# Kernel tuning notes

Hardware: AMD Instinct MI355X
Metric: run time of the kernel (lower is better)

Reference implementation:

```python
import jax, jax.numpy as jnp
import numpy as np

DECAY = 0.99
EPS = 1e-5
BETA = 0.25

def _l2norm(v, axis=-1):
    # F.normalize: x / max(||x||, 1e-12)
    n = jnp.sqrt(jnp.sum(v * v, axis=axis, keepdims=True))
    return v / jnp.maximum(n, 1e-12)

def setup_inputs() -> dict:
    key = jax.random.key(0)
    k0, k1, k2, k3 = jax.random.split(key, 4)
    B, C, H, W, E, K = 8, 256, 64, 64, 32, 8192
    x = jax.random.normal(k0, (B, C, H, W), jnp.float32)
    Wq = jax.random.normal(k1, (E, C), jnp.float32) * 0.05  # 1x1 conv kernel
    bq = jnp.zeros((E,), jnp.float32)
    emb = jax.random.normal(k2, (K, E), jnp.float32)
    emb = _l2norm(emb, axis=1)  # matches F.normalize init in __init__
    ema_cluster_size = jnp.ones((K,), jnp.float32)
    ema_weight = emb  # consistent post-init EMA state
    return {"x": x, "Wq": Wq, "bq": bq, "embedding": emb,
            "ema_cluster_size": ema_cluster_size, "ema_weight": ema_weight}

def reference(x, Wq, bq, embedding, ema_cluster_size, ema_weight):
    B, C, H, W = x.shape
    E = Wq.shape[0]
    K = embedding.shape[0]
    # quant_conv: 1x1 conv == per-pixel linear
    z = jnp.einsum('bchw,ec->behw', x, Wq) + bq[None, :, None, None]  # [B,E,H,W]
    z_flat = z.transpose(0, 2, 3, 1).reshape(-1, E)  # [N,E]
    # get_idx(use_znorm=True): cosine similarity argmax (== argmin L2 on normalized)
    zn = _l2norm(z_flat, axis=1)
    en = _l2norm(embedding, axis=1)
    indices = jnp.argmax(zn @ en.T, axis=1)  # [N]
    # codebook gather (raw embedding, as in torch)
    z_q = embedding[indices].reshape(B, H, W, E).transpose(0, 3, 1, 2)  # [B,E,H,W]
    # EMA update (training path; scatter == one-hot.T @ z_flat / one-hot.sum)
    counts = jax.ops.segment_sum(jnp.ones((z_flat.shape[0],), z_flat.dtype), indices, num_segments=K)
    dw = jax.ops.segment_sum(z_flat, indices, num_segments=K)  # [K,E]
    new_cs = DECAY * ema_cluster_size + (1.0 - DECAY) * counts
    new_w = DECAY * ema_weight + (1.0 - DECAY) * dw
    n = jnp.sum(new_cs)
    cs_smoothed = (new_cs + EPS) / (n + K * EPS) * n
    new_embedding = new_w / cs_smoothed[:, None]
    # commitment loss + straight-through
    qloss = BETA * jnp.mean((jax.lax.stop_gradient(z_q) - z) ** 2)
    z_q_st = z + jax.lax.stop_gradient(z_q - z)
    return (z_q_st, indices.reshape(B, H, W), qloss, new_embedding, new_cs, new_w)
```

## Files before the change

kernel.cpp:

```cpp
#include <hip/hip_runtime.h>

#define B_ 8
#define C_ 256
#define HW_ 4096
#define E_ 32
#define K_ 8192
#define N_ 32768
#define NCHUNK 4
#define KC_ (K_ / NCHUNK)
#define NSTAGE (KC_ / 128)
#define KSEG 32

#define DECAY_ 0.99f
#define OMD_   0.01f
#define EPS_   1e-5f
#define BETA_  0.25f

#define O_ZQ   0
#define O_IDX  1048576
#define O_QL   1081344
#define O_NEMB 1081345
#define O_NCS  1343489
#define O_NW   1351681

#define WS_EH   0u
#define WS_EM   131072u
#define WS_Z    262144u
#define WS_PACK 1310720u
#define WS_CNT  1572864u
#define WS_DW   1581056u
#define WS_SCAL 1843200u

typedef float f32x4 __attribute__((ext_vector_type(4)));
typedef short s16x8 __attribute__((ext_vector_type(8)));
typedef unsigned long long u64;

__device__ __forceinline__ unsigned short f2bf(float f) {
    unsigned u = __float_as_uint(f);
    u = u + 0x7fffu + ((u >> 16) & 1u);
    return (unsigned short)(u >> 16);
}
__device__ __forceinline__ float bf2f(unsigned short h) {
    return __uint_as_float(((unsigned)h) << 16);
}
__device__ __forceinline__ unsigned ford(float f) {
    unsigned u = __float_as_uint(f);
    return (u & 0x80000000u) ? ~u : (u | 0x80000000u);
}
__device__ __forceinline__ int imax(int a, int b) { return a > b ? a : b; }
__device__ __forceinline__ int imin(int a, int b) { return a < b ? a : b; }

__device__ __forceinline__ void gload_lds16(const void* g, void* l) {
    __builtin_amdgcn_global_load_lds(
        (const __attribute__((address_space(1))) unsigned int*)g,
        (__attribute__((address_space(3))) unsigned int*)l, 16, 0, 0);
}

__global__ __launch_bounds__(256) void k_norm_split(const float* __restrict__ emb,
                                                    uint4* __restrict__ eh16,
                                                    uint4* __restrict__ em16) {
    int k = blockIdx.x * 256 + threadIdx.x;
    if (k >= K_) return;
    const float4* r = (const float4*)(emb + (size_t)k * E_);
    float v[E_];
    float ss = 0.f;
#pragma unroll
    for (int i = 0; i < 8; i++) {
        float4 t = r[i];
        v[i*4+0] = t.x; v[i*4+1] = t.y; v[i*4+2] = t.z; v[i*4+3] = t.w;
        ss += t.x*t.x + t.y*t.y + t.z*t.z + t.w*t.w;
    }
    float inv = 1.0f / fmaxf(sqrtf(ss), 1e-12f);
    unsigned short h1a[E_], h2a[E_];
#pragma unroll
    for (int e = 0; e < E_; e++) {
        float en = v[e] * inv;
        unsigned short h1 = f2bf(en);
        float r1 = en - bf2f(h1);
        h1a[e] = h1; h2a[e] = f2bf(r1);
    }
    int t = k >> 4, c15 = k & 15;
#pragma unroll
    for (int i = 0; i < 4; i++) {
        eh16[t * 64 + i * 16 + c15] = ((uint4*)h1a)[i];
        em16[t * 64 + i * 16 + c15] = ((uint4*)h2a)[i];
    }
}

__global__ __launch_bounds__(512) void k_z(const float* __restrict__ x,
                                           const float* __restrict__ Wq,
                                           const float* __restrict__ bq,
                                           float* __restrict__ zout) {
    __shared__ float wqt[C_ * E_];
    int tid = threadIdx.x;
#pragma unroll
    for (int i = 0; i < 16; i++) {
        int g = i * 512 + tid;
        int e = g >> 8;
        int c = g & 255;
        wqt[c * E_ + e] = Wq[g];
    }
    __syncthreads();
    int lp = tid & 63, eg = tid >> 6;
    int n0 = blockIdx.x * 64 + lp;
    int b  = n0 >> 12, hw = n0 & (HW_ - 1);
    const float* xp = x + (size_t)b * C_ * HW_ + hw;
    float a0 = 0.f, a1 = 0.f, a2 = 0.f, a3 = 0.f;
#pragma unroll 4
    for (int c = 0; c < C_; c++) {
        float xv = xp[(size_t)c * HW_];
        float4 wv = *(const float4*)(wqt + c * E_ + eg * 4);
        a0 += xv * wv.x; a1 += xv * wv.y; a2 += xv * wv.z; a3 += xv * wv.w;
    }
    float4 o = make_float4(a0 + bq[eg*4+0], a1 + bq[eg*4+1],
                           a2 + bq[eg*4+2], a3 + bq[eg*4+3]);
    *(float4*)(zout + (size_t)n0 * E_ + eg * 4) = o;
}

__global__ __launch_bounds__(256, 4) void k_score_mfma(const float* __restrict__ zws,
                                                       const char* __restrict__ ehb,
                                                       const char* __restrict__ emb_b,
                                                       int2* __restrict__ pk2) {
    __shared__ __align__(16) char smem[32768];

    int tid  = threadIdx.x;
    int lane = tid & 63;
    int w    = tid >> 6;
    int chunk = blockIdx.y;

    s16x8 a1, a2;
    {
        int ploc = w * 16 + (lane & 15);
        int n0   = blockIdx.x * 64 + ploc;
        int e0   = (lane >> 4) * 8;
        const float4* zp = (const float4*)(zws + (size_t)n0 * E_ + e0);
        float4 z0 = zp[0], z1 = zp[1];
        float zz[8] = {z0.x, z0.y, z0.z, z0.w, z1.x, z1.y, z1.z, z1.w};
#pragma unroll
        for (int j = 0; j < 8; j++) {
            float zv = zz[j] * 134217728.0f;
            unsigned short h1 = f2bf(zv);
            float r1 = zv - bf2f(h1);
            a1[j] = (short)h1; a2[j] = (short)f2bf(r1);
        }
    }

    const char* srcp[4];
#pragma unroll
    for (int i = 0; i < 4; i++) {
        int d = i * 256 + tid;
        int pl = d >> 9, dd = d & 511;
        srcp[i] = (pl ? emb_b : ehb) + (size_t)chunk * (KC_ * 64) + dd * 16;
    }

#pragma unroll
    for (int i = 0; i < 4; i++)
        gload_lds16(srcp[i], smem + (i * 256 + tid) * 16);
    __syncthreads();

    int rbase = 8191 - chunk * KC_ - (lane & 15);
    int bq1[4], bq2[4];
#pragma unroll
    for (int j = 0; j < 4; j++) { bq1[j] = (int)0x80000000; bq2[j] = (int)0x80000000; }
    f32x4 zero4 = {0.f, 0.f, 0.f, 0.f};

    for (int st = 0; st < NSTAGE; st++) {
        if (st + 1 < NSTAGE) {
            char* dst = smem + ((st + 1) & 1) * 16384;
#pragma unroll
            for (int i = 0; i < 4; i++)
                gload_lds16(srcp[i] + (size_t)(st + 1) * 8192, dst + (i * 256 + tid) * 16);
        }
        const char* cur = smem + (st & 1) * 16384;
        int rst = rbase - st * 128;

#pragma unroll
        for (int g = 0; g < 2; g++) {
            int ct = g * 4;
            s16x8 b1[4], b2[4];
#pragma unroll
            for (int q = 0; q < 4; q++) {
                b1[q] = ((const s16x8*)(cur +        (ct + q) * 1024))[lane];
                b2[q] = ((const s16x8*)(cur + 8192 + (ct + q) * 1024))[lane];
            }
            f32x4 acc[4];
#pragma unroll
            for (int q = 0; q < 4; q++)
                acc[q] = __builtin_amdgcn_mfma_f32_16x16x32_bf16(a1, b1[q], zero4, 0, 0, 0);
#pragma unroll
            for (int q = 0; q < 4; q++)
                acc[q] = __builtin_amdgcn_mfma_f32_16x16x32_bf16(a1, b2[q], acc[q], 0, 0, 0);
#pragma unroll
            for (int q = 0; q < 4; q++)
                acc[q] = __builtin_amdgcn_mfma_f32_16x16x32_bf16(a2, b1[q], acc[q], 0, 0, 0);
            int r0 = rst - ct * 16;
#pragma unroll
            for (int j = 0; j < 4; j++) {
                int v0 = ((int)acc[0][j] & (int)0xFFFFE000) | r0;
                int v1 = ((int)acc[1][j] & (int)0xFFFFE000) | (r0 - 16);
                int v2 = ((int)acc[2][j] & (int)0xFFFFE000) | (r0 - 32);
                int v3 = ((int)acc[3][j] & (int)0xFFFFE000) | (r0 - 48);
                int hi = imax(imax(v0, v1), imax(v2, v3));
                int m  = imin(bq1[j], hi);
                bq1[j] = imax(bq1[j], hi);
                bq2[j] = imax(bq2[j], m);
            }
        }
        __syncthreads();
    }

#pragma unroll
    for (int off = 1; off < 16; off <<= 1) {
#pragma unroll
        for (int j = 0; j < 4; j++) {
            int o1 = __shfl_xor(bq1[j], off, 64);
            int o2 = __shfl_xor(bq2[j], off, 64);
            int m  = imin(bq1[j], o1);
            bq1[j] = imax(bq1[j], o1);
            bq2[j] = imax(imax(bq2[j], o2), m);
        }
    }
    if ((lane & 15) == 0) {
        int rowbase = blockIdx.x * 64 + w * 16 + (lane >> 4) * 4;
#pragma unroll
        for (int j = 0; j < 4; j++)
            pk2[(size_t)chunk * N_ + rowbase + j] = make_int2(bq1[j], bq2[j]);
    }
}

__device__ __forceinline__ float rescore(const float* __restrict__ emb, int k,
                                         const float* zrow) {
    const float4* r = (const float4*)(emb + (size_t)k * E_);
    float4 v[8];
    float ss = 0.f;
#pragma unroll
    for (int i = 0; i < 8; i++) {
        v[i] = r[i];
        ss += v[i].x * v[i].x + v[i].y * v[i].y + v[i].z * v[i].z + v[i].w * v[i].w;
    }
    float inv = 1.0f / fmaxf(sqrtf(ss), 1e-12f);
    const float4* zp = (const float4*)zrow;
    float sx = 0.f, sy = 0.f, sz = 0.f, sw = 0.f;
#pragma unroll
    for (int i = 0; i < 8; i++) {
        float4 e4 = make_float4(v[i].x * inv, v[i].y * inv, v[i].z * inv, v[i].w * inv);
        float4 zr = zp[i];
        sx += zr.x * e4.x; sy += zr.y * e4.y;
        sz += zr.z * e4.z; sw += zr.w * e4.w;
    }
    return (sx + sy) + (sz + sw);
}

__global__ __launch_bounds__(256) void k_scatter(const float* __restrict__ zws,
                                                 const int2* __restrict__ pk2,
                                                 const float* __restrict__ emb,
                                                 float* __restrict__ out_zq,
                                                 float* __restrict__ out_idx,
                                                 float* __restrict__ scal) {
    __shared__ float zbuf[64 * E_];
    __shared__ int   idxs_s[64];
    __shared__ float red[4];
    int tid = threadIdx.x;

    const float4* zsrc = (const float4*)(zws + (size_t)blockIdx.x * 64 * E_);
    float4* zdst = (float4*)zbuf;
    zdst[tid]       = zsrc[tid];
    zdst[tid + 256] = zsrc[tid + 256];
    __syncthreads();

    {
        int p = tid >> 2, c4 = tid & 3;
        int nn = blockIdx.x * 64 + p;
        int2 c2 = pk2[(size_t)c4 * N_ + nn];
        u64 pkd = 0;
#pragma unroll
        for (int t = 0; t < 2; t++) {
            int raw = t ? c2.y : c2.x;
            int k = 8191 - (raw & 0x1fff);
            k = k < 0 ? 0 : (k > K_ - 1 ? K_ - 1 : k);
            float s = rescore(emb, k, zbuf + p * E_);
            u64 pk = ((u64)ford(s) << 32) | (unsigned)(K_ - 1 - k);
            pkd = pkd > pk ? pkd : pk;
        }
        u64 o = __shfl_xor(pkd, 1, 64); pkd = pkd > o ? pkd : o;
        o = __shfl_xor(pkd, 2, 64);     pkd = pkd > o ? pkd : o;
        if (c4 == 0) {
            int bi = K_ - 1 - (int)(unsigned)(pkd & 0xffffffffu);
            idxs_s[p] = bi;
            out_idx[nn] = (float)bi;
        }
    }
    __syncthreads();

    int lp = tid & 63, eg = tid >> 6;
    int n  = blockIdx.x * 64 + lp;
    int b  = n >> 12, hw = n & (HW_ - 1);
    int idx = idxs_s[lp];
    const float* er = emb + (size_t)idx * E_ + eg * 8;
    float* o = out_zq + (size_t)b * E_ * HW_ + (size_t)(eg * 8) * HW_ + hw;

    float sq = 0.f;
#pragma unroll
    for (int j = 0; j < 8; j++) {
        float zv = zbuf[lp * E_ + eg * 8 + j];
        float qf = er[j];
        float d = qf - zv;
        sq += d * d;
        o[(size_t)j * HW_] = qf;
    }

#pragma unroll
    for (int off = 32; off > 0; off >>= 1) sq += __shfl_down(sq, off);
    int lane = tid & 63, wid = tid >> 6;
    if (lane == 0) red[wid] = sq;
    __syncthreads();
    if (tid == 0) atomicAdd(scal + 1, red[0] + red[1] + red[2] + red[3]);
}

__global__ __launch_bounds__(256) void k_dw(const float* __restrict__ zws,
                                            const float* __restrict__ idxf,
                                            float* __restrict__ dw,
                                            float* __restrict__ cnt) {
    __shared__ float acc[KSEG * E_];
    __shared__ int   cnt_s[KSEG];
    int tid = threadIdx.x;
    int kbase = blockIdx.x * KSEG;

#pragma unroll
    for (int i = 0; i < KSEG * E_ / 256; i++) acc[tid + i * 256] = 0.f;
    if (tid < KSEG) cnt_s[tid] = 0;
    __syncthreads();

    const float4* idx4 = (const float4*)idxf;
#pragma unroll 2
    for (int it = 0; it < N_ / 1024; ++it) {
        float4 f = idx4[it * 256 + tid];
        int n0 = (it * 256 + tid) * 4;
        int ii[4] = {(int)f.x, (int)f.y, (int)f.z, (int)f.w};
#pragma unroll
        for (int s = 0; s < 4; s++) {
            unsigned d = (unsigned)(ii[s] - kbase);
            if (d < (unsigned)KSEG) {
                const float4* zr = (const float4*)(zws + (size_t)(n0 + s) * E_);
                float* ap = acc + d * E_;
#pragma unroll
                for (int j = 0; j < 8; j++) {
                    float4 v = zr[j];
                    atomicAdd(ap + j * 4 + 0, v.x);
                    atomicAdd(ap + j * 4 + 1, v.y);
                    atomicAdd(ap + j * 4 + 2, v.z);
                    atomicAdd(ap + j * 4 + 3, v.w);
                }
                atomicAdd(cnt_s + d, 1);
            }
        }
    }
    __syncthreads();

#pragma unroll
    for (int i = 0; i < KSEG * E_ / 256; i++)
        dw[(size_t)kbase * E_ + tid + i * 256] = acc[tid + i * 256];
    if (tid < KSEG) cnt[kbase + tid] = (float)cnt_s[tid];
}

__global__ __launch_bounds__(256) void k_ema_cs(const float* __restrict__ cs,
                                                const float* __restrict__ cnt,
                                                float* __restrict__ out_ncs,
                                                float* __restrict__ scal) {
    int tid = threadIdx.x;
    int k = blockIdx.x * 256 + tid;
    float v = DECAY_ * cs[k] + OMD_ * cnt[k];
    out_ncs[k] = v;

    float s = v;
#pragma unroll
    for (int off = 32; off > 0; off >>= 1) s += __shfl_down(s, off);
    __shared__ float red[4];
    int lane = tid & 63, wid = tid >> 6;
    if (lane == 0) red[wid] = s;
    __syncthreads();
    if (tid == 0) atomicAdd(scal + 0, red[0] + red[1] + red[2] + red[3]);
}

__global__ __launch_bounds__(256) void k_final(const float* __restrict__ ew,
                                               const float* __restrict__ dw,
                                               const float* __restrict__ cs,
                                               const float* __restrict__ cnt,
                                               const float* __restrict__ scal,
                                               float* __restrict__ out_nw,
                                               float* __restrict__ out_nemb,
                                               float* __restrict__ out_ql) {
    int j = blockIdx.x * 256 + threadIdx.x;
    float v = DECAY_ * ew[j] + OMD_ * dw[j];
    out_nw[j] = v;
    float nsum = scal[0];
    int k = j >> 5;
    float csk = DECAY_ * cs[k] + OMD_ * cnt[k];
    float denom = (csk + EPS_) / (nsum + (float)K_ * EPS_) * nsum;
    out_nemb[j] = v / denom;
    if (j == 0) {
        out_ql[0] = BETA_ * scal[1] / (float)(B_ * E_ * HW_);
    }
}

extern "C" void kernel_launch(void* const* d_in, const int* in_sizes, int n_in,
                              void* d_out, int out_size, void* d_ws, size_t ws_size,
                              hipStream_t stream) {
    const float* x   = (const float*)d_in[0];
    const float* Wq  = (const float*)d_in[1];
    const float* bq  = (const float*)d_in[2];
    const float* emb = (const float*)d_in[3];
    const float* cs  = (const float*)d_in[4];
    const float* ew  = (const float*)d_in[5];
    float* out = (float*)d_out;
    float* ws  = (float*)d_ws;

    hipMemsetAsync(ws + WS_SCAL, 0, 2 * sizeof(float), stream);

    k_norm_split<<<K_ / 256, 256, 0, stream>>>(emb,
        (uint4*)(ws + WS_EH), (uint4*)(ws + WS_EM));
    k_z<<<N_ / 64, 512, 0, stream>>>(x, Wq, bq, ws + WS_Z);
    k_score_mfma<<<dim3(N_ / 64, NCHUNK), 256, 0, stream>>>(ws + WS_Z,
        (const char*)(ws + WS_EH), (const char*)(ws + WS_EM),
        (int2*)(ws + WS_PACK));
    k_scatter<<<N_ / 64, 256, 0, stream>>>(ws + WS_Z,
        (const int2*)(ws + WS_PACK), emb,
        out + O_ZQ, out + O_IDX, ws + WS_SCAL);
    k_dw<<<K_ / KSEG, 256, 0, stream>>>(ws + WS_Z, out + O_IDX,
                                        ws + WS_DW, ws + WS_CNT);
    k_ema_cs<<<K_ / 256, 256, 0, stream>>>(cs, ws + WS_CNT, out + O_NCS, ws + WS_SCAL);
    k_final<<<(K_ * E_) / 256, 256, 0, stream>>>(ew, ws + WS_DW, cs, ws + WS_CNT,
                                                 ws + WS_SCAL, out + O_NW,
                                                 out + O_NEMB, out + O_QL);
}
```

Before: 218.6 us.

## Enlarge score blocks to 512 threads, fold EMA cluster-size kernel into others

The scoring kernel now uses 512-thread blocks covering 128 pixels, so each staged codebook tile in shared memory is reused by twice as many waves and half as many blocks reload it. The separate EMA cluster-size kernel is removed. The sum of new cluster sizes is computed analytically from the sum of old sizes, accumulated in the norm kernel, plus the total pixel count, and k_final now writes the new cluster sizes. The norm kernel is also split across four threads per codebook row for more parallelism. Risks are lower occupancy from the larger blocks and tiny float differences in the analytic sum.

```diff
diff --git a/kernel.cpp b/kernel.cpp
--- a/kernel.cpp
+++ b/kernel.cpp
@@ -10,6 +10,7 @@
 #define KC_ (K_ / NCHUNK)
 #define NSTAGE (KC_ / 128)
 #define KSEG 32
+#define PIX 128
 
 #define DECAY_ 0.99f
 #define OMD_   0.01f
@@ -57,33 +58,38 @@
 }
 
 __global__ __launch_bounds__(256) void k_norm_split(const float* __restrict__ emb,
+                                                    const float* __restrict__ cs,
                                                     uint4* __restrict__ eh16,
-                                                    uint4* __restrict__ em16) {
-    int k = blockIdx.x * 256 + threadIdx.x;
-    if (k >= K_) return;
-    const float4* r = (const float4*)(emb + (size_t)k * E_);
-    float v[E_];
-    float ss = 0.f;
-#pragma unroll
-    for (int i = 0; i < 8; i++) {
-        float4 t = r[i];
-        v[i*4+0] = t.x; v[i*4+1] = t.y; v[i*4+2] = t.z; v[i*4+3] = t.w;
-        ss += t.x*t.x + t.y*t.y + t.z*t.z + t.w*t.w;
-    }
+                                                    uint4* __restrict__ em16,
+                                                    float* __restrict__ scal) {
+    int t4 = blockIdx.x * 256 + threadIdx.x;
+    int k = t4 >> 2, q = t4 & 3;
+    const float4* r = (const float4*)(emb + (size_t)k * E_ + q * 8);
+    float4 u0 = r[0], u1 = r[1];
+    float ss = u0.x*u0.x + u0.y*u0.y + u0.z*u0.z + u0.w*u0.w
+             + u1.x*u1.x + u1.y*u1.y + u1.z*u1.z + u1.w*u1.w;
+    ss += __shfl_xor(ss, 1, 64);
+    ss += __shfl_xor(ss, 2, 64);
     float inv = 1.0f / fmaxf(sqrtf(ss), 1e-12f);
-    unsigned short h1a[E_], h2a[E_];
-#pragma unroll
-    for (int e = 0; e < E_; e++) {
+
+    float v[8] = {u0.x, u0.y, u0.z, u0.w, u1.x, u1.y, u1.z, u1.w};
+    unsigned short h1a[8], h2a[8];
+#pragma unroll
+    for (int e = 0; e < 8; e++) {
         float en = v[e] * inv;
         unsigned short h1 = f2bf(en);
         float r1 = en - bf2f(h1);
         h1a[e] = h1; h2a[e] = f2bf(r1);
     }
     int t = k >> 4, c15 = k & 15;
-#pragma unroll
-    for (int i = 0; i < 4; i++) {
-        eh16[t * 64 + i * 16 + c15] = ((uint4*)h1a)[i];
-        em16[t * 64 + i * 16 + c15] = ((uint4*)h2a)[i];
+    eh16[t * 64 + q * 16 + c15] = ((uint4*)h1a)[0];
+    em16[t * 64 + q * 16 + c15] = ((uint4*)h2a)[0];
+
+    if (threadIdx.x < 64) {
+        float cv = cs[blockIdx.x * 64 + threadIdx.x];
+#pragma unroll
+        for (int off = 32; off > 0; off >>= 1) cv += __shfl_down(cv, off);
+        if (threadIdx.x == 0) atomicAdd(scal + 0, cv);
     }
 }
 
@@ -117,7 +123,7 @@
     *(float4*)(zout + (size_t)n0 * E_ + eg * 4) = o;
 }
 
-__global__ __launch_bounds__(256, 4) void k_score_mfma(const float* __restrict__ zws,
+__global__ __launch_bounds__(512, 8) void k_score_mfma(const float* __restrict__ zws,
                                                        const char* __restrict__ ehb,
                                                        const char* __restrict__ emb_b,
                                                        int2* __restrict__ pk2) {
@@ -131,7 +137,7 @@
     s16x8 a1, a2;
     {
         int ploc = w * 16 + (lane & 15);
-        int n0   = blockIdx.x * 64 + ploc;
+        int n0   = blockIdx.x * PIX + ploc;
         int e0   = (lane >> 4) * 8;
         const float4* zp = (const float4*)(zws + (size_t)n0 * E_ + e0);
         float4 z0 = zp[0], z1 = zp[1];
@@ -145,17 +151,17 @@
         }
     }
 
-    const char* srcp[4];
-#pragma unroll
-    for (int i = 0; i < 4; i++) {
-        int d = i * 256 + tid;
+    const char* srcp[2];
+#pragma unroll
+    for (int i = 0; i < 2; i++) {
+        int d = i * 512 + tid;
         int pl = d >> 9, dd = d & 511;
         srcp[i] = (pl ? emb_b : ehb) + (size_t)chunk * (KC_ * 64) + dd * 16;
     }
 
 #pragma unroll
-    for (int i = 0; i < 4; i++)
-        gload_lds16(srcp[i], smem + (i * 256 + tid) * 16);
+    for (int i = 0; i < 2; i++)
+        gload_lds16(srcp[i], smem + (i * 512 + tid) * 16);
     __syncthreads();
 
     int rbase = 8191 - chunk * KC_ - (lane & 15);
@@ -168,8 +174,8 @@
         if (st + 1 < NSTAGE) {
             char* dst = smem + ((st + 1) & 1) * 16384;
 #pragma unroll
-            for (int i = 0; i < 4; i++)
-                gload_lds16(srcp[i] + (size_t)(st + 1) * 8192, dst + (i * 256 + tid) * 16);
+            for (int i = 0; i < 2; i++)
+                gload_lds16(srcp[i] + (size_t)(st + 1) * 8192, dst + (i * 512 + tid) * 16);
         }
         const char* cur = smem + (st & 1) * 16384;
         int rst = rbase - st * 128;
@@ -221,7 +227,7 @@
         }
     }
     if ((lane & 15) == 0) {
-        int rowbase = blockIdx.x * 64 + w * 16 + (lane >> 4) * 4;
+        int rowbase = blockIdx.x * PIX + w * 16 + (lane >> 4) * 4;
 #pragma unroll
         for (int j = 0; j < 4; j++)
             pk2[(size_t)chunk * N_ + rowbase + j] = make_int2(bq1[j], bq2[j]);
@@ -363,25 +369,6 @@
     if (tid < KSEG) cnt[kbase + tid] = (float)cnt_s[tid];
 }
 
-__global__ __launch_bounds__(256) void k_ema_cs(const float* __restrict__ cs,
-                                                const float* __restrict__ cnt,
-                                                float* __restrict__ out_ncs,
-                                                float* __restrict__ scal) {
-    int tid = threadIdx.x;
-    int k = blockIdx.x * 256 + tid;
-    float v = DECAY_ * cs[k] + OMD_ * cnt[k];
-    out_ncs[k] = v;
-
-    float s = v;
-#pragma unroll
-    for (int off = 32; off > 0; off >>= 1) s += __shfl_down(s, off);
-    __shared__ float red[4];
-    int lane = tid & 63, wid = tid >> 6;
-    if (lane == 0) red[wid] = s;
-    __syncthreads();
-    if (tid == 0) atomicAdd(scal + 0, red[0] + red[1] + red[2] + red[3]);
-}
-
 __global__ __launch_bounds__(256) void k_final(const float* __restrict__ ew,
                                                const float* __restrict__ dw,
                                                const float* __restrict__ cs,
@@ -389,15 +376,17 @@
                                                const float* __restrict__ scal,
                                                float* __restrict__ out_nw,
                                                float* __restrict__ out_nemb,
+                                               float* __restrict__ out_ncs,
                                                float* __restrict__ out_ql) {
     int j = blockIdx.x * 256 + threadIdx.x;
     float v = DECAY_ * ew[j] + OMD_ * dw[j];
     out_nw[j] = v;
-    float nsum = scal[0];
+    float nsum = DECAY_ * scal[0] + OMD_ * (float)N_;
     int k = j >> 5;
     float csk = DECAY_ * cs[k] + OMD_ * cnt[k];
     float denom = (csk + EPS_) / (nsum + (float)K_ * EPS_) * nsum;
     out_nemb[j] = v / denom;
+    if ((j & 31) == 0) out_ncs[k] = csk;
     if (j == 0) {
         out_ql[0] = BETA_ * scal[1] / (float)(B_ * E_ * HW_);
     }
@@ -417,10 +406,10 @@
 
     hipMemsetAsync(ws + WS_SCAL, 0, 2 * sizeof(float), stream);
 
-    k_norm_split<<<K_ / 256, 256, 0, stream>>>(emb,
-        (uint4*)(ws + WS_EH), (uint4*)(ws + WS_EM));
+    k_norm_split<<<K_ * 4 / 256, 256, 0, stream>>>(emb, cs,
+        (uint4*)(ws + WS_EH), (uint4*)(ws + WS_EM), ws + WS_SCAL);
     k_z<<<N_ / 64, 512, 0, stream>>>(x, Wq, bq, ws + WS_Z);
-    k_score_mfma<<<dim3(N_ / 64, NCHUNK), 256, 0, stream>>>(ws + WS_Z,
+    k_score_mfma<<<dim3(N_ / PIX, NCHUNK), 512, 0, stream>>>(ws + WS_Z,
         (const char*)(ws + WS_EH), (const char*)(ws + WS_EM),
         (int2*)(ws + WS_PACK));
     k_scatter<<<N_ / 64, 256, 0, stream>>>(ws + WS_Z,
@@ -428,8 +417,8 @@
         out + O_ZQ, out + O_IDX, ws + WS_SCAL);
     k_dw<<<K_ / KSEG, 256, 0, stream>>>(ws + WS_Z, out + O_IDX,
                                         ws + WS_DW, ws + WS_CNT);
-    k_ema_cs<<<K_ / 256, 256, 0, stream>>>(cs, ws + WS_CNT, out + O_NCS, ws + WS_SCAL);
     k_final<<<(K_ * E_) / 256, 256, 0, stream>>>(ew, ws + WS_DW, cs, ws + WS_CNT,
                                                  ws + WS_SCAL, out + O_NW,
-                                                 out + O_NEMB, out + O_QL);
-}
+                                                 out + O_NEMB, out + O_NCS,
+                                                 out + O_QL);
+}
```

Measured after the change: 280.7 us. 1.28x slower.
